# Performance work log

Measured on AMD Instinct MI355X. Metric: run time of the kernel, lower is better.

Reference implementation:

```python
import jax, jax.numpy as jnp
import numpy as np
from jax.scipy.special import logsumexp

T = 2048   # trajectory length
S = 512    # state dim (self.s)
B = 16     # number of options (self.b)
A = 18     # number of actions (self.a)
PEN = 0.5  # abstract_penalty
NEG = -1e9 # padding log-prob for not-yet-created option rows


def setup_inputs() -> dict:
    key = jax.random.key(0)
    k1, k2, k3, k4, k5 = jax.random.split(key, 5)
    s_i = jax.random.normal(k1, (T + 1, S), dtype=jnp.float32)
    W_action = jax.random.normal(k2, (S, B * A), dtype=jnp.float32) * 0.05
    W_stop = jax.random.normal(k3, (S, B * 2), dtype=jnp.float32) * 0.05
    W_start = jax.random.normal(k4, (S, B), dtype=jnp.float32) * 0.05
    actions = jax.random.randint(k5, (T,), 0, A, dtype=jnp.int64)
    return {"s_i": s_i, "W_action": W_action, "W_stop": W_stop,
            "W_start": W_start, "actions": actions}


def _hmm_logp(s_i, W_action, W_stop, W_start, actions):
    # abstract_policy_net: linear heads + log_softmax over the relevant axis
    action_logps = jax.nn.log_softmax((s_i @ W_action).reshape(T + 1, B, A), axis=-1)
    stop_logps = jax.nn.log_softmax((s_i @ W_stop).reshape(T + 1, B, 2), axis=-1)
    start_logps = jax.nn.log_softmax(s_i @ W_start, axis=-1)  # (T+1, B)

    # padded option_step_dist buffer: row i is created at step i (torch.cat append)
    buf0 = jnp.full((T, B), NEG, dtype=s_i.dtype).at[0].set(start_logps[0])

    def step(carry, xs):
        buf, tot = carry
        i, act = xs
        stop = stop_logps[i]          # (B, 2)
        start_lps = start_logps[i]    # (B,)
        # rearrange mass: options that stop get redistributed to new starts
        total_rearrange = logsumexp(buf + stop[:, 1]) - PEN
        new_mass = start_lps + total_rearrange
        buf2 = (buf + stop[:, 0]).at[i].set(new_mass)
        buf = jnp.where(i > 0, buf2, buf)  # i == 0 skips the rearrange branch
        action_lps = action_logps[i, :, act]  # (B,)
        tot = tot + logsumexp(action_lps + buf)
        return (buf, tot), None

    xs = (jnp.arange(T), actions)
    (buf, total_logp), _ = jax.lax.scan(step, (buf0, jnp.asarray(0.0, s_i.dtype)), xs)
    # final: all options must stop (note original uses index 0 here, as in source)
    total_logp = total_logp + logsumexp(stop_logps[-1, :, 0] + buf)
    return total_logp


def reference(s_i, W_action, W_stop, W_start, actions):
    return _hmm_logp(s_i, W_action, W_stop, W_start, actions)
```

## Files before the change

### kernel.cpp

```cpp
#include <hip/hip_runtime.h>

#define TT    2048
#define SS    512
#define NB    16
#define EPEN  0.60653065971263342f
#define NCHUNK 64
#define CLEN   32

typedef __attribute__((ext_vector_type(4))) float  floatx4;
typedef __attribute__((ext_vector_type(8))) short  bf16x8;

__device__ __forceinline__ ushort f2bf(float x) {
  unsigned u = __float_as_uint(x);
  u += 0x7fffu + ((u >> 16) & 1u);
  return (ushort)(u >> 16);
}

__device__ __forceinline__ unsigned pack2(ushort a, ushort b) {
  return (unsigned)a | ((unsigned)b << 16);
}

__global__ __launch_bounds__(256) void prep_kernel(
    const float* __restrict__ Wa, const float* __restrict__ Ws,
    const float* __restrict__ Wst, const float* __restrict__ s_i,
    ushort* __restrict__ Wt2, ushort* __restrict__ Af)
{
  int fid = blockIdx.x * 256 + threadIdx.x;
  if (fid < 21504) {
    const int q = fid & 3, rc = (fid >> 2) & 15, kt = (fid >> 6) & 15, colt = fid >> 10;
    const int col = colt * 16 + rc;
    const int kbase = kt * 32 + q * 8;
    ushort h[8];
    #pragma unroll
    for (int e = 0; e < 8; ++e) {
      const int k = kbase + e;
      float v;
      if (col < 288)      v = Wa [(size_t)k * 288 + col];
      else if (col < 320) v = Ws [(size_t)k * 32  + (col - 288)];
      else                v = Wst[(size_t)k * 16  + (col - 320)];
      h[e] = f2bf(v);
    }
    uint4 o = make_uint4(pack2(h[0], h[1]), pack2(h[2], h[3]),
                         pack2(h[4], h[5]), pack2(h[6], h[7]));
    *(uint4*)(Wt2 + (size_t)fid * 8) = o;
  } else {
    const int aid = fid - 21504;
    if (aid < 132096) {
      const int q = aid & 3, rc = (aid >> 2) & 15, kt = (aid >> 6) & 15, mt = aid >> 10;
      int row = mt * 16 + rc; if (row > TT) row = TT;
      const float* src = s_i + (size_t)row * SS + kt * 32 + q * 8;
      float4 v0 = *(const float4*)src;
      float4 v1 = *(const float4*)(src + 4);
      uint4 o = make_uint4(pack2(f2bf(v0.x), f2bf(v0.y)),
                           pack2(f2bf(v0.z), f2bf(v0.w)),
                           pack2(f2bf(v1.x), f2bf(v1.y)),
                           pack2(f2bf(v1.z), f2bf(v1.w)));
      *(uint4*)(Af + (size_t)aid * 8) = o;
    }
  }
}

__global__ __launch_bounds__(512) void proj_kernel(
    const ushort* __restrict__ Af,
    const ushort* __restrict__ Wt2,
    const int*   __restrict__ actions,
    float4*      __restrict__ coef)
{
  __shared__ float lg[16][346];

  const int tid  = threadIdx.x;
  const int wave = tid >> 6, lane = tid & 63;
  const int q = lane >> 4, rc = lane & 15;
  const int row0 = blockIdx.x * 16;

  const int kh = wave >> 2;
  const int ng = wave & 3;
  const int ntiles = (ng == 0) ? 6 : 5;
  const int kt0 = kh * 8;

  const ushort* aBase = Af  + (size_t)blockIdx.x * 8192 + rc * 32 + q * 8;
  const ushort* bBase = Wt2 + rc * 32 + q * 8;

  floatx4 acc[6];
  #pragma unroll
  for (int j = 0; j < 6; ++j) acc[j] = (floatx4)(0.f);

  bf16x8 aC, aN, bC[6], bN[6];

  aC = *(const bf16x8*)(aBase + kt0 * 512);
  #pragma unroll
  for (int j = 0; j < 6; ++j) {
    if (j < ntiles) {
      const int colt = ng + 4 * j;
      bC[j] = *(const bf16x8*)(bBase + (size_t)colt * 8192 + kt0 * 512);
    }
  }

  #pragma unroll
  for (int kk = 0; kk < 8; ++kk) {
    const int kt = kt0 + kk;
    if (kk < 7) {
      aN = *(const bf16x8*)(aBase + (kt + 1) * 512);
      #pragma unroll
      for (int j = 0; j < 6; ++j) {
        if (j < ntiles) {
          const int colt = ng + 4 * j;
          bN[j] = *(const bf16x8*)(bBase + (size_t)colt * 8192 + (kt + 1) * 512);
        }
      }
    }
    #pragma unroll
    for (int j = 0; j < 6; ++j) {
      if (j < ntiles)
        acc[j] = __builtin_amdgcn_mfma_f32_16x16x32_bf16(aC, bC[j], acc[j], 0, 0, 0);
    }
    aC = aN;
    #pragma unroll
    for (int j = 0; j < 6; ++j) {
      if (j < ntiles) bC[j] = bN[j];
    }
  }

  if (kh == 0) {
    #pragma unroll
    for (int j = 0; j < 6; ++j) {
      if (j < ntiles) {
        const int colt = ng + 4 * j;
        #pragma unroll
        for (int reg = 0; reg < 4; ++reg)
          lg[q * 4 + reg][colt * 16 + rc] = acc[j][reg];
      }
    }
  }
  __syncthreads();
  if (kh == 1) {
    #pragma unroll
    for (int j = 0; j < 6; ++j) {
      if (j < ntiles) {
        const int colt = ng + 4 * j;
        #pragma unroll
        for (int reg = 0; reg < 4; ++reg)
          lg[q * 4 + reg][colt * 16 + rc] += acc[j][reg];
      }
    }
  }
  __syncthreads();

  if (tid < 256) {
    const int r = tid >> 4, b = tid & 15;
    const int row = row0 + r;
    if (row < TT) {
      float m = -3.4e38f;
      #pragma unroll
      for (int a = 0; a < 18; ++a) m = fmaxf(m, lg[r][b * 18 + a]);
      float sum = 0.f;
      #pragma unroll
      for (int a = 0; a < 18; ++a) sum += __expf(lg[r][b * 18 + a] - m);
      int act = actions[row];
      float aprob = __expf(lg[r][b * 18 + act] - m) / sum;

      float x0 = lg[r][288 + 2 * b], x1 = lg[r][288 + 2 * b + 1];
      float mm = fmaxf(x0, x1);
      float e0 = __expf(x0 - mm), e1 = __expf(x1 - mm);
      float inv = 1.f / (e0 + e1);

      float ms = -3.4e38f;
      #pragma unroll
      for (int j = 0; j < 16; ++j) ms = fmaxf(ms, lg[r][320 + j]);
      float ssum = 0.f;
      #pragma unroll
      for (int j = 0; j < 16; ++j) ssum += __expf(lg[r][320 + j] - ms);
      float stp = __expf(lg[r][320 + b] - ms) / ssum;

      coef[(size_t)row * NB + b] = make_float4(e0 * inv, e1 * inv, stp, aprob);
    } else if (row == TT) {
      float x0 = lg[r][288 + 2 * b], x1 = lg[r][288 + 2 * b + 1];
      float mm = fmaxf(x0, x1);
      float e0 = __expf(x0 - mm), e1 = __expf(x1 - mm);
      coef[(size_t)TT * NB + b] = make_float4(1.f, 0.f, 0.f, e0 / (e0 + e1));
    }
  }
}

__global__ __launch_bounds__(64) void pass1_kernel(
    const float4* __restrict__ coef,
    float* __restrict__ Wws, float* __restrict__ Mws)
{
  const int chunk = blockIdx.x * 4 + (threadIdx.x >> 4);
  const int c = threadIdx.x & 15;
  const int i0 = chunk * CLEN + 1;

  float G[16];
  #pragma unroll
  for (int r = 0; r < 16; ++r) G[r] = (r == c) ? 1.f : 0.f;

  float4 cfA[16], cfB[16];
  #pragma unroll
  for (int r = 0; r < 16; ++r) cfA[r] = coef[(size_t)i0 * 16 + r];
  #pragma unroll
  for (int r = 0; r < 16; ++r) cfB[r] = coef[(size_t)(i0 + 1) * 16 + r];

#define P1BODY(CUR, NXT, J)                                                  \
  {                                                                          \
    if ((J) + 2 < CLEN) {                                                    \
      _Pragma("unroll")                                                      \
      for (int r = 0; r < 16; ++r)                                           \
        NXT[r] = coef[(size_t)(i0 + (J) + 2) * 16 + r];                      \
    }                                                                        \
    float ta = 0.f, tb = 0.f, tc = 0.f, td = 0.f;                            \
    _Pragma("unroll")                                                        \
    for (int r = 0; r < 4; ++r) {                                            \
      ta = fmaf(CUR[r].y,      G[r],      ta);                               \
      tb = fmaf(CUR[r + 4].y,  G[r + 4],  tb);                               \
      tc = fmaf(CUR[r + 8].y,  G[r + 8],  tc);                               \
      td = fmaf(CUR[r + 12].y, G[r + 12], td);                               \
    }                                                                        \
    float et = EPEN * ((ta + tb) + (tc + td));                               \
    _Pragma("unroll")                                                        \
    for (int r = 0; r < 16; ++r)                                             \
      G[r] = fmaf(CUR[r].x, G[r], CUR[r].z * et);                            \
    float wa = 0.f, wb = 0.f, wc = 0.f, wd = 0.f;                            \
    _Pragma("unroll")                                                        \
    for (int r = 0; r < 4; ++r) {                                            \
      wa = fmaf(CUR[r].w,      G[r],      wa);                               \
      wb = fmaf(CUR[r + 4].w,  G[r + 4],  wb);                               \
      wc = fmaf(CUR[r + 8].w,  G[r + 8],  wc);                               \
      wd = fmaf(CUR[r + 12].w, G[r + 12], wd);                               \
    }                                                                        \
    Wws[(size_t)(chunk * CLEN + (J)) * 16 + c] = (wa + wb) + (wc + wd);      \
  }

  for (int j = 0; j < CLEN; j += 2) {
    P1BODY(cfA, cfB, j);
    P1BODY(cfB, cfA, j + 1);
  }
#undef P1BODY

  #pragma unroll
  for (int r = 0; r < 16; ++r)
    Mws[chunk * 256 + r * 16 + c] = G[r];
}

__global__ __launch_bounds__(512) void pass2_kernel(
    const float4* __restrict__ coef,
    const float* __restrict__ Wws, const float* __restrict__ Mws,
    float* __restrict__ out)
{
  __shared__ float pbuf[NCHUNK][16];
  __shared__ float wacc[8];

  const int tid = threadIdx.x;
  long long Ktot = 0;

  if (tid < 64) {
    const int r = tid >> 2, g = tid & 3;
    float pj0 = coef[4 * g + 0].z;
    float pj1 = coef[4 * g + 1].z;
    float pj2 = coef[4 * g + 2].z;
    float pj3 = coef[4 * g + 3].z;

    const int moff = r * 16 + 4 * g;
    const int gb0 = 64 * g, gb1 = gb0 + 16, gb2 = gb0 + 32, gb3 = gb0 + 48;
    int Ecum = 0;

    float4 mR0 = *(const float4*)&Mws[0 * 256 + moff];
    float4 mR1 = *(const float4*)&Mws[1 * 256 + moff];
    float4 mR2 = *(const float4*)&Mws[2 * 256 + moff];
    float4 mR3 = *(const float4*)&Mws[3 * 256 + moff];
    float4 mR4 = *(const float4*)&Mws[4 * 256 + moff];
    float4 mR5 = *(const float4*)&Mws[5 * 256 + moff];
    float4 mR6 = *(const float4*)&Mws[6 * 256 + moff];
    float4 mR7 = *(const float4*)&Mws[7 * 256 + moff];

#define P2BODY(K, MREG, KPF)                                                 \
    {                                                                        \
      if (r == 0)                                                            \
        *(float4*)&pbuf[(K)][4 * g] = make_float4(pj0, pj1, pj2, pj3);       \
      Ktot += 32LL * (long long)Ecum;                                        \
      float part = fmaf(MREG.x, pj0,                                         \
                   fmaf(MREG.y, pj1, fmaf(MREG.z, pj2, MREG.w * pj3)));      \
      if ((KPF) < NCHUNK)                                                    \
        MREG = *(const float4*)&Mws[(KPF) * 256 + moff];                     \
              \
      part += __int_as_float(__builtin_amdgcn_mov_dpp(                       \
          __float_as_int(part), 0x39, 0xF, 0xF, true));      \
      part += __int_as_float(__builtin_amdgcn_mov_dpp(                       \
          __float_as_int(part), 0x4E, 0xF, 0xF, true));      \
      int ip = __float_as_int(part);                                         \
      float n0 = __int_as_float(__builtin_amdgcn_ds_bpermute(gb0, ip));      \
      float n1 = __int_as_float(__builtin_amdgcn_ds_bpermute(gb1, ip));      \
      float n2 = __int_as_float(__builtin_amdgcn_ds_bpermute(gb2, ip));      \
      float n3 = __int_as_float(__builtin_amdgcn_ds_bpermute(gb3, ip));      \
      int y0b = __builtin_amdgcn_readfirstlane(__float_as_int(n0));          \
      int eb = (y0b >> 23) & 255;                                            \
      Ecum += eb - 127;                                                      \
      float sc = __int_as_float((254 - eb) << 23);                           \
      pj0 = n0 * sc; pj1 = n1 * sc; pj2 = n2 * sc; pj3 = n3 * sc;            \
    }

    for (int kb = 0; kb < NCHUNK; kb += 8) {
      P2BODY(kb + 0, mR0, kb + 8);
      P2BODY(kb + 1, mR1, kb + 9);
      P2BODY(kb + 2, mR2, kb + 10);
      P2BODY(kb + 3, mR3, kb + 11);
      P2BODY(kb + 4, mR4, kb + 12);
      P2BODY(kb + 5, mR5, kb + 13);
      P2BODY(kb + 6, mR6, kb + 14);
      P2BODY(kb + 7, mR7, kb + 15);
    }
#undef P2BODY
  }
  __syncthreads();

  const int j0 = tid * 4;
  const int chunk = j0 >> 5;
  float p[16];
  #pragma unroll
  for (int c = 0; c < 16; ++c) p[c] = pbuf[chunk][c];

  float lacc = 0.f;
  #pragma unroll
  for (int jj = 0; jj < 4; ++jj) {
    const float* w = Wws + (size_t)(j0 + jj) * 16;
    float4 w0 = *(const float4*)(w);
    float4 w1 = *(const float4*)(w + 4);
    float4 w2 = *(const float4*)(w + 8);
    float4 w3 = *(const float4*)(w + 12);
    float s0 = fmaf(w0.x, p[0],  fmaf(w0.y, p[1],  fmaf(w0.z, p[2],  w0.w * p[3])));
    float s1 = fmaf(w1.x, p[4],  fmaf(w1.y, p[5],  fmaf(w1.z, p[6],  w1.w * p[7])));
    float s2 = fmaf(w2.x, p[8],  fmaf(w2.y, p[9],  fmaf(w2.z, p[10], w2.w * p[11])));
    float s3 = fmaf(w3.x, p[12], fmaf(w3.y, p[13], fmaf(w3.z, p[14], w3.w * p[15])));
    lacc += __logf((s0 + s1) + (s2 + s3));
  }

  if (tid == 0) {
    float U0 = 0.f;
    #pragma unroll
    for (int c = 0; c < 16; ++c) U0 = fmaf(coef[c].w, coef[c].z, U0);
    lacc += __logf(U0);
  }

  lacc += __shfl_xor(lacc, 1, 64);
  lacc += __shfl_xor(lacc, 2, 64);
  lacc += __shfl_xor(lacc, 4, 64);
  lacc += __shfl_xor(lacc, 8, 64);
  lacc += __shfl_xor(lacc, 16, 64);
  lacc += __shfl_xor(lacc, 32, 64);
  if ((tid & 63) == 0) wacc[tid >> 6] = lacc;
  __syncthreads();
  if (tid == 0) {
    double s = 0.0;
    #pragma unroll
    for (int i = 0; i < 8; ++i) s += (double)wacc[i];
    out[0] = (float)(s + 0.6931471805599453 * (double)Ktot);
  }
}

extern "C" void kernel_launch(void* const* d_in, const int* in_sizes, int n_in,
                              void* d_out, int out_size, void* d_ws, size_t ws_size,
                              hipStream_t stream) {
  const float* s_i = (const float*)d_in[0];
  const float* Wa  = (const float*)d_in[1];
  const float* Ws  = (const float*)d_in[2];
  const float* Wst = (const float*)d_in[3];
  const int*   act = (const int*)d_in[4];

  char* ws = (char*)d_ws;
  float4* coef = (float4*)ws;
  float*  Wws  = (float*)(ws + 524544);
  float*  Mws  = (float*)(ws + 524544 + 131072);
  ushort* Wt2  = (ushort*)(ws + 721152);
  ushort* Af   = (ushort*)(ws + 1065216);

  prep_kernel <<<600, 256, 0, stream>>>(Wa, Ws, Wst, s_i, Wt2, Af);
  proj_kernel <<<129, 512, 0, stream>>>(Af, Wt2, act, coef);
  pass1_kernel<<<16,  64,  0, stream>>>(coef, Wws, Mws);
  pass2_kernel<<<1,   512, 0, stream>>>(coef, Wws, Mws, (float*)d_out);
}
```

Measured before the change: 98.11 us.

## Fuse four kernels into one cooperative kernel with grid-wide syncs

Merges the prep, projection, pass1 and pass2 kernels into a single cooperative launch of 129 blocks, with grid.sync() separating the stages. The aim is to remove the per-kernel launch gaps between four small dependent kernels. In exchange, the prep stage now runs on fewer threads in a grid-stride loop, and each stage pays for a grid barrier. Cooperative launch also needs all blocks to be resident at once, which limits occupancy and the available shared memory per block.

```diff
diff --git a/kernel.cpp b/kernel.cpp
--- a/kernel.cpp
+++ b/kernel.cpp
@@ -1,4 +1,7 @@
 #include <hip/hip_runtime.h>
+#include <hip/hip_cooperative_groups.h>
+
+namespace cg = cooperative_groups;
 
 #define TT    2048
 #define SS    512
@@ -20,32 +23,44 @@
   return (unsigned)a | ((unsigned)b << 16);
 }
 
-__global__ __launch_bounds__(256) void prep_kernel(
-    const float* __restrict__ Wa, const float* __restrict__ Ws,
+__global__ __launch_bounds__(512) void mega_kernel(
+    const float* __restrict__ Wa,  const float* __restrict__ Ws,
     const float* __restrict__ Wst, const float* __restrict__ s_i,
-    ushort* __restrict__ Wt2, ushort* __restrict__ Af)
+    const int*   __restrict__ actions,
+    ushort* __restrict__ Wt2, ushort* __restrict__ Af,
+    float4* __restrict__ coef,
+    float*  __restrict__ Wws, float* __restrict__ Mws,
+    float*  __restrict__ out)
 {
-  int fid = blockIdx.x * 256 + threadIdx.x;
-  if (fid < 21504) {
-    const int q = fid & 3, rc = (fid >> 2) & 15, kt = (fid >> 6) & 15, colt = fid >> 10;
-    const int col = colt * 16 + rc;
-    const int kbase = kt * 32 + q * 8;
-    ushort h[8];
-    #pragma unroll
-    for (int e = 0; e < 8; ++e) {
-      const int k = kbase + e;
-      float v;
-      if (col < 288)      v = Wa [(size_t)k * 288 + col];
-      else if (col < 320) v = Ws [(size_t)k * 32  + (col - 288)];
-      else                v = Wst[(size_t)k * 16  + (col - 320)];
-      h[e] = f2bf(v);
-    }
-    uint4 o = make_uint4(pack2(h[0], h[1]), pack2(h[2], h[3]),
-                         pack2(h[4], h[5]), pack2(h[6], h[7]));
-    *(uint4*)(Wt2 + (size_t)fid * 8) = o;
-  } else {
-    const int aid = fid - 21504;
-    if (aid < 132096) {
+  cg::grid_group grid = cg::this_grid();
+
+  __shared__ float lg[16][346];
+  __shared__ float pbuf[NCHUNK][16];
+  __shared__ float wacc[8];
+
+  const int tid = threadIdx.x;
+  const int bid = blockIdx.x;
+
+  for (int fid = bid * 512 + tid; fid < 153600; fid += 129 * 512) {
+    if (fid < 21504) {
+      const int q = fid & 3, rc = (fid >> 2) & 15, kt = (fid >> 6) & 15, colt = fid >> 10;
+      const int col = colt * 16 + rc;
+      const int kbase = kt * 32 + q * 8;
+      ushort h[8];
+      #pragma unroll
+      for (int e = 0; e < 8; ++e) {
+        const int k = kbase + e;
+        float v;
+        if (col < 288)      v = Wa [(size_t)k * 288 + col];
+        else if (col < 320) v = Ws [(size_t)k * 32  + (col - 288)];
+        else                v = Wst[(size_t)k * 16  + (col - 320)];
+        h[e] = f2bf(v);
+      }
+      uint4 o = make_uint4(pack2(h[0], h[1]), pack2(h[2], h[3]),
+                           pack2(h[4], h[5]), pack2(h[6], h[7]));
+      *(uint4*)(Wt2 + (size_t)fid * 8) = o;
+    } else {
+      const int aid = fid - 21504;
       const int q = aid & 3, rc = (aid >> 2) & 15, kt = (aid >> 6) & 15, mt = aid >> 10;
       int row = mt * 16 + rc; if (row > TT) row = TT;
       const float* src = s_i + (size_t)row * SS + kt * 32 + q * 8;
@@ -58,301 +73,284 @@
       *(uint4*)(Af + (size_t)aid * 8) = o;
     }
   }
-}
-
-__global__ __launch_bounds__(512) void proj_kernel(
-    const ushort* __restrict__ Af,
-    const ushort* __restrict__ Wt2,
-    const int*   __restrict__ actions,
-    float4*      __restrict__ coef)
-{
-  __shared__ float lg[16][346];
-
-  const int tid  = threadIdx.x;
-  const int wave = tid >> 6, lane = tid & 63;
-  const int q = lane >> 4, rc = lane & 15;
-  const int row0 = blockIdx.x * 16;
-
-  const int kh = wave >> 2;
-  const int ng = wave & 3;
-  const int ntiles = (ng == 0) ? 6 : 5;
-  const int kt0 = kh * 8;
-
-  const ushort* aBase = Af  + (size_t)blockIdx.x * 8192 + rc * 32 + q * 8;
-  const ushort* bBase = Wt2 + rc * 32 + q * 8;
-
-  floatx4 acc[6];
-  #pragma unroll
-  for (int j = 0; j < 6; ++j) acc[j] = (floatx4)(0.f);
-
-  bf16x8 aC, aN, bC[6], bN[6];
-
-  aC = *(const bf16x8*)(aBase + kt0 * 512);
-  #pragma unroll
-  for (int j = 0; j < 6; ++j) {
-    if (j < ntiles) {
-      const int colt = ng + 4 * j;
-      bC[j] = *(const bf16x8*)(bBase + (size_t)colt * 8192 + kt0 * 512);
-    }
-  }
-
-  #pragma unroll
-  for (int kk = 0; kk < 8; ++kk) {
-    const int kt = kt0 + kk;
-    if (kk < 7) {
-      aN = *(const bf16x8*)(aBase + (kt + 1) * 512);
+  grid.sync();
+
+  {
+    const int wave = tid >> 6, lane = tid & 63;
+    const int q = lane >> 4, rc = lane & 15;
+    const int row0 = bid * 16;
+
+    const int kh = wave >> 2;
+    const int ng = wave & 3;
+    const int ntiles = (ng == 0) ? 6 : 5;
+    const int kt0 = kh * 8;
+
+    const ushort* aBase = Af  + (size_t)bid * 8192 + rc * 32 + q * 8;
+    const ushort* bBase = Wt2 + rc * 32 + q * 8;
+
+    floatx4 acc[6];
+    #pragma unroll
+    for (int j = 0; j < 6; ++j) acc[j] = (floatx4)(0.f);
+
+    bf16x8 aC, aN, bC[6], bN[6];
+
+    aC = *(const bf16x8*)(aBase + kt0 * 512);
+    #pragma unroll
+    for (int j = 0; j < 6; ++j) {
+      if (j < ntiles) {
+        const int colt = ng + 4 * j;
+        bC[j] = *(const bf16x8*)(bBase + (size_t)colt * 8192 + kt0 * 512);
+      }
+    }
+
+    #pragma unroll
+    for (int kk = 0; kk < 8; ++kk) {
+      const int kt = kt0 + kk;
+      if (kk < 7) {
+        aN = *(const bf16x8*)(aBase + (kt + 1) * 512);
+        #pragma unroll
+        for (int j = 0; j < 6; ++j) {
+          if (j < ntiles) {
+            const int colt = ng + 4 * j;
+            bN[j] = *(const bf16x8*)(bBase + (size_t)colt * 8192 + (kt + 1) * 512);
+          }
+        }
+      }
+      #pragma unroll
+      for (int j = 0; j < 6; ++j) {
+        if (j < ntiles)
+          acc[j] = __builtin_amdgcn_mfma_f32_16x16x32_bf16(aC, bC[j], acc[j], 0, 0, 0);
+      }
+      aC = aN;
+      #pragma unroll
+      for (int j = 0; j < 6; ++j) {
+        if (j < ntiles) bC[j] = bN[j];
+      }
+    }
+
+    if (kh == 0) {
       #pragma unroll
       for (int j = 0; j < 6; ++j) {
         if (j < ntiles) {
           const int colt = ng + 4 * j;
-          bN[j] = *(const bf16x8*)(bBase + (size_t)colt * 8192 + (kt + 1) * 512);
+          #pragma unroll
+          for (int reg = 0; reg < 4; ++reg)
+            lg[q * 4 + reg][colt * 16 + rc] = acc[j][reg];
         }
       }
     }
-    #pragma unroll
-    for (int j = 0; j < 6; ++j) {
-      if (j < ntiles)
-        acc[j] = __builtin_amdgcn_mfma_f32_16x16x32_bf16(aC, bC[j], acc[j], 0, 0, 0);
-    }
-    aC = aN;
-    #pragma unroll
-    for (int j = 0; j < 6; ++j) {
-      if (j < ntiles) bC[j] = bN[j];
+    __syncthreads();
+    if (kh == 1) {
+      #pragma unroll
+      for (int j = 0; j < 6; ++j) {
+        if (j < ntiles) {
+          const int colt = ng + 4 * j;
+          #pragma unroll
+          for (int reg = 0; reg < 4; ++reg)
+            lg[q * 4 + reg][colt * 16 + rc] += acc[j][reg];
+        }
+      }
+    }
+    __syncthreads();
+
+    if (tid < 256) {
+      const int r = tid >> 4, b = tid & 15;
+      const int row = row0 + r;
+      if (row < TT) {
+        float m = -3.4e38f;
+        #pragma unroll
+        for (int a = 0; a < 18; ++a) m = fmaxf(m, lg[r][b * 18 + a]);
+        float sum = 0.f;
+        #pragma unroll
+        for (int a = 0; a < 18; ++a) sum += __expf(lg[r][b * 18 + a] - m);
+        int act = actions[row];
+        float aprob = __expf(lg[r][b * 18 + act] - m) / sum;
+
+        float x0 = lg[r][288 + 2 * b], x1 = lg[r][288 + 2 * b + 1];
+        float mm = fmaxf(x0, x1);
+        float e0 = __expf(x0 - mm), e1 = __expf(x1 - mm);
+        float inv = 1.f / (e0 + e1);
+
+        float ms = -3.4e38f;
+        #pragma unroll
+        for (int j = 0; j < 16; ++j) ms = fmaxf(ms, lg[r][320 + j]);
+        float ssum = 0.f;
+        #pragma unroll
+        for (int j = 0; j < 16; ++j) ssum += __expf(lg[r][320 + j] - ms);
+        float stp = __expf(lg[r][320 + b] - ms) / ssum;
+
+        coef[(size_t)row * NB + b] = make_float4(e0 * inv, e1 * inv, stp, aprob);
+      } else if (row == TT) {
+        float x0 = lg[r][288 + 2 * b], x1 = lg[r][288 + 2 * b + 1];
+        float mm = fmaxf(x0, x1);
+        float e0 = __expf(x0 - mm), e1 = __expf(x1 - mm);
+        coef[(size_t)TT * NB + b] = make_float4(1.f, 0.f, 0.f, e0 / (e0 + e1));
+      }
     }
   }
-
-  if (kh == 0) {
-    #pragma unroll
-    for (int j = 0; j < 6; ++j) {
-      if (j < ntiles) {
-        const int colt = ng + 4 * j;
-        #pragma unroll
-        for (int reg = 0; reg < 4; ++reg)
-          lg[q * 4 + reg][colt * 16 + rc] = acc[j][reg];
-      }
-    }
-  }
-  __syncthreads();
-  if (kh == 1) {
-    #pragma unroll
-    for (int j = 0; j < 6; ++j) {
-      if (j < ntiles) {
-        const int colt = ng + 4 * j;
-        #pragma unroll
-        for (int reg = 0; reg < 4; ++reg)
-          lg[q * 4 + reg][colt * 16 + rc] += acc[j][reg];
-      }
-    }
-  }
-  __syncthreads();
-
-  if (tid < 256) {
-    const int r = tid >> 4, b = tid & 15;
-    const int row = row0 + r;
-    if (row < TT) {
-      float m = -3.4e38f;
-      #pragma unroll
-      for (int a = 0; a < 18; ++a) m = fmaxf(m, lg[r][b * 18 + a]);
-      float sum = 0.f;
-      #pragma unroll
-      for (int a = 0; a < 18; ++a) sum += __expf(lg[r][b * 18 + a] - m);
-      int act = actions[row];
-      float aprob = __expf(lg[r][b * 18 + act] - m) / sum;
-
-      float x0 = lg[r][288 + 2 * b], x1 = lg[r][288 + 2 * b + 1];
-      float mm = fmaxf(x0, x1);
-      float e0 = __expf(x0 - mm), e1 = __expf(x1 - mm);
-      float inv = 1.f / (e0 + e1);
-
-      float ms = -3.4e38f;
-      #pragma unroll
-      for (int j = 0; j < 16; ++j) ms = fmaxf(ms, lg[r][320 + j]);
-      float ssum = 0.f;
-      #pragma unroll
-      for (int j = 0; j < 16; ++j) ssum += __expf(lg[r][320 + j] - ms);
-      float stp = __expf(lg[r][320 + b] - ms) / ssum;
-
-      coef[(size_t)row * NB + b] = make_float4(e0 * inv, e1 * inv, stp, aprob);
-    } else if (row == TT) {
-      float x0 = lg[r][288 + 2 * b], x1 = lg[r][288 + 2 * b + 1];
-      float mm = fmaxf(x0, x1);
-      float e0 = __expf(x0 - mm), e1 = __expf(x1 - mm);
-      coef[(size_t)TT * NB + b] = make_float4(1.f, 0.f, 0.f, e0 / (e0 + e1));
-    }
-  }
-}
-
-__global__ __launch_bounds__(64) void pass1_kernel(
-    const float4* __restrict__ coef,
-    float* __restrict__ Wws, float* __restrict__ Mws)
-{
-  const int chunk = blockIdx.x * 4 + (threadIdx.x >> 4);
-  const int c = threadIdx.x & 15;
-  const int i0 = chunk * CLEN + 1;
-
-  float G[16];
-  #pragma unroll
-  for (int r = 0; r < 16; ++r) G[r] = (r == c) ? 1.f : 0.f;
-
-  float4 cfA[16], cfB[16];
-  #pragma unroll
-  for (int r = 0; r < 16; ++r) cfA[r] = coef[(size_t)i0 * 16 + r];
-  #pragma unroll
-  for (int r = 0; r < 16; ++r) cfB[r] = coef[(size_t)(i0 + 1) * 16 + r];
+  grid.sync();
+
+  if (bid < 16 && tid < 64) {
+    const int chunk = bid * 4 + (tid >> 4);
+    const int c = tid & 15;
+    const int i0 = chunk * CLEN + 1;
+
+    float G[16];
+    #pragma unroll
+    for (int r = 0; r < 16; ++r) G[r] = (r == c) ? 1.f : 0.f;
+
+    float4 cfA[16], cfB[16];
+    #pragma unroll
+    for (int r = 0; r < 16; ++r) cfA[r] = coef[(size_t)i0 * 16 + r];
+    #pragma unroll
+    for (int r = 0; r < 16; ++r) cfB[r] = coef[(size_t)(i0 + 1) * 16 + r];
 
 #define P1BODY(CUR, NXT, J)                                                  \
-  {                                                                          \
-    if ((J) + 2 < CLEN) {                                                    \
+    {                                                                        \
+      if ((J) + 2 < CLEN) {                                                  \
+        _Pragma("unroll")                                                    \
+        for (int r = 0; r < 16; ++r)                                         \
+          NXT[r] = coef[(size_t)(i0 + (J) + 2) * 16 + r];                    \
+      }                                                                      \
+      float ta = 0.f, tb = 0.f, tc = 0.f, td = 0.f;                          \
+      _Pragma("unroll")                                                      \
+      for (int r = 0; r < 4; ++r) {                                          \
+        ta = fmaf(CUR[r].y,      G[r],      ta);                             \
+        tb = fmaf(CUR[r + 4].y,  G[r + 4],  tb);                             \
+        tc = fmaf(CUR[r + 8].y,  G[r + 8],  tc);                             \
+        td = fmaf(CUR[r + 12].y, G[r + 12], td);                             \
+      }                                                                      \
+      float et = EPEN * ((ta + tb) + (tc + td));                             \
       _Pragma("unroll")                                                      \
       for (int r = 0; r < 16; ++r)                                           \
-        NXT[r] = coef[(size_t)(i0 + (J) + 2) * 16 + r];                      \
-    }                                                                        \
-    float ta = 0.f, tb = 0.f, tc = 0.f, td = 0.f;                            \
-    _Pragma("unroll")                                                        \
-    for (int r = 0; r < 4; ++r) {                                            \
-      ta = fmaf(CUR[r].y,      G[r],      ta);                               \
-      tb = fmaf(CUR[r + 4].y,  G[r + 4],  tb);                               \
-      tc = fmaf(CUR[r + 8].y,  G[r + 8],  tc);                               \
-      td = fmaf(CUR[r + 12].y, G[r + 12], td);                               \
-    }                                                                        \
-    float et = EPEN * ((ta + tb) + (tc + td));                               \
-    _Pragma("unroll")                                                        \
-    for (int r = 0; r < 16; ++r)                                             \
-      G[r] = fmaf(CUR[r].x, G[r], CUR[r].z * et);                            \
-    float wa = 0.f, wb = 0.f, wc = 0.f, wd = 0.f;                            \
-    _Pragma("unroll")                                                        \
-    for (int r = 0; r < 4; ++r) {                                            \
-      wa = fmaf(CUR[r].w,      G[r],      wa);                               \
-      wb = fmaf(CUR[r + 4].w,  G[r + 4],  wb);                               \
-      wc = fmaf(CUR[r + 8].w,  G[r + 8],  wc);                               \
-      wd = fmaf(CUR[r + 12].w, G[r + 12], wd);                               \
-    }                                                                        \
-    Wws[(size_t)(chunk * CLEN + (J)) * 16 + c] = (wa + wb) + (wc + wd);      \
+        G[r] = fmaf(CUR[r].x, G[r], CUR[r].z * et);                          \
+      float wa = 0.f, wb = 0.f, wc = 0.f, wd = 0.f;                          \
+      _Pragma("unroll")                                                      \
+      for (int r = 0; r < 4; ++r) {                                          \
+        wa = fmaf(CUR[r].w,      G[r],      wa);                             \
+        wb = fmaf(CUR[r + 4].w,  G[r + 4],  wb);                             \
+        wc = fmaf(CUR[r + 8].w,  G[r + 8],  wc);                             \
+        wd = fmaf(CUR[r + 12].w, G[r + 12], wd);                             \
+      }                                                                      \
+      Wws[(size_t)(chunk * CLEN + (J)) * 16 + c] = (wa + wb) + (wc + wd);    \
+    }
+
+    for (int j = 0; j < CLEN; j += 2) {
+      P1BODY(cfA, cfB, j);
+      P1BODY(cfB, cfA, j + 1);
+    }
+#undef P1BODY
+
+    #pragma unroll
+    for (int r = 0; r < 16; ++r)
+      Mws[chunk * 256 + r * 16 + c] = G[r];
   }
-
-  for (int j = 0; j < CLEN; j += 2) {
-    P1BODY(cfA, cfB, j);
-    P1BODY(cfB, cfA, j + 1);
-  }
-#undef P1BODY
-
-  #pragma unroll
-  for (int r = 0; r < 16; ++r)
-    Mws[chunk * 256 + r * 16 + c] = G[r];
-}
-
-__global__ __launch_bounds__(512) void pass2_kernel(
-    const float4* __restrict__ coef,
-    const float* __restrict__ Wws, const float* __restrict__ Mws,
-    float* __restrict__ out)
-{
-  __shared__ float pbuf[NCHUNK][16];
-  __shared__ float wacc[8];
-
-  const int tid = threadIdx.x;
-  long long Ktot = 0;
-
-  if (tid < 64) {
-    const int r = tid >> 2, g = tid & 3;
-    float pj0 = coef[4 * g + 0].z;
-    float pj1 = coef[4 * g + 1].z;
-    float pj2 = coef[4 * g + 2].z;
-    float pj3 = coef[4 * g + 3].z;
-
-    const int moff = r * 16 + 4 * g;
-    const int gb0 = 64 * g, gb1 = gb0 + 16, gb2 = gb0 + 32, gb3 = gb0 + 48;
-    int Ecum = 0;
-
-    float4 mR0 = *(const float4*)&Mws[0 * 256 + moff];
-    float4 mR1 = *(const float4*)&Mws[1 * 256 + moff];
-    float4 mR2 = *(const float4*)&Mws[2 * 256 + moff];
-    float4 mR3 = *(const float4*)&Mws[3 * 256 + moff];
-    float4 mR4 = *(const float4*)&Mws[4 * 256 + moff];
-    float4 mR5 = *(const float4*)&Mws[5 * 256 + moff];
-    float4 mR6 = *(const float4*)&Mws[6 * 256 + moff];
-    float4 mR7 = *(const float4*)&Mws[7 * 256 + moff];
+  grid.sync();
+
+  if (bid == 0) {
+    long long Ktot = 0;
+
+    if (tid < 64) {
+      const int r = tid >> 2, g = tid & 3;
+      float pj0 = coef[4 * g + 0].z;
+      float pj1 = coef[4 * g + 1].z;
+      float pj2 = coef[4 * g + 2].z;
+      float pj3 = coef[4 * g + 3].z;
+
+      const int moff = r * 16 + 4 * g;
+      const int gb0 = 64 * g, gb1 = gb0 + 16, gb2 = gb0 + 32, gb3 = gb0 + 48;
+      int Ecum = 0;
+
+      float4 mR0 = *(const float4*)&Mws[0 * 256 + moff];
+      float4 mR1 = *(const float4*)&Mws[1 * 256 + moff];
+      float4 mR2 = *(const float4*)&Mws[2 * 256 + moff];
+      float4 mR3 = *(const float4*)&Mws[3 * 256 + moff];
+      float4 mR4 = *(const float4*)&Mws[4 * 256 + moff];
+      float4 mR5 = *(const float4*)&Mws[5 * 256 + moff];
+      float4 mR6 = *(const float4*)&Mws[6 * 256 + moff];
+      float4 mR7 = *(const float4*)&Mws[7 * 256 + moff];
 
 #define P2BODY(K, MREG, KPF)                                                 \
-    {                                                                        \
-      if (r == 0)                                                            \
-        *(float4*)&pbuf[(K)][4 * g] = make_float4(pj0, pj1, pj2, pj3);       \
-      Ktot += 32LL * (long long)Ecum;                                        \
-      float part = fmaf(MREG.x, pj0,                                         \
-                   fmaf(MREG.y, pj1, fmaf(MREG.z, pj2, MREG.w * pj3)));      \
-      if ((KPF) < NCHUNK)                                                    \
-        MREG = *(const float4*)&Mws[(KPF) * 256 + moff];                     \
-              \
-      part += __int_as_float(__builtin_amdgcn_mov_dpp(                       \
-          __float_as_int(part), 0x39, 0xF, 0xF, true));      \
-      part += __int_as_float(__builtin_amdgcn_mov_dpp(                       \
-          __float_as_int(part), 0x4E, 0xF, 0xF, true));      \
-      int ip = __float_as_int(part);                                         \
-      float n0 = __int_as_float(__builtin_amdgcn_ds_bpermute(gb0, ip));      \
-      float n1 = __int_as_float(__builtin_amdgcn_ds_bpermute(gb1, ip));      \
-      float n2 = __int_as_float(__builtin_amdgcn_ds_bpermute(gb2, ip));      \
-      float n3 = __int_as_float(__builtin_amdgcn_ds_bpermute(gb3, ip));      \
-      int y0b = __builtin_amdgcn_readfirstlane(__float_as_int(n0));          \
-      int eb = (y0b >> 23) & 255;                                            \
-      Ecum += eb - 127;                                                      \
-      float sc = __int_as_float((254 - eb) << 23);                           \
-      pj0 = n0 * sc; pj1 = n1 * sc; pj2 = n2 * sc; pj3 = n3 * sc;            \
-    }
-
-    for (int kb = 0; kb < NCHUNK; kb += 8) {
-      P2BODY(kb + 0, mR0, kb + 8);
-      P2BODY(kb + 1, mR1, kb + 9);
-      P2BODY(kb + 2, mR2, kb + 10);
-      P2BODY(kb + 3, mR3, kb + 11);
-      P2BODY(kb + 4, mR4, kb + 12);
-      P2BODY(kb + 5, mR5, kb + 13);
-      P2BODY(kb + 6, mR6, kb + 14);
-      P2BODY(kb + 7, mR7, kb + 15);
-    }
+      {                                                                      \
+        if (r == 0)                                                          \
+          *(float4*)&pbuf[(K)][4 * g] = make_float4(pj0, pj1, pj2, pj3);     \
+        Ktot += 32LL * (long long)Ecum;                                      \
+        float part = fmaf(MREG.x, pj0,                                       \
+                     fmaf(MREG.y, pj1, fmaf(MREG.z, pj2, MREG.w * pj3)));    \
+        if ((KPF) < NCHUNK)                                                  \
+          MREG = *(const float4*)&Mws[(KPF) * 256 + moff];                   \
+        part += __int_as_float(__builtin_amdgcn_mov_dpp(                     \
+            __float_as_int(part), 0x39, 0xF, 0xF, true));    \
+        part += __int_as_float(__builtin_amdgcn_mov_dpp(                     \
+            __float_as_int(part), 0x4E, 0xF, 0xF, true));    \
+        int ip = __float_as_int(part);                                       \
+        float n0 = __int_as_float(__builtin_amdgcn_ds_bpermute(gb0, ip));    \
+        float n1 = __int_as_float(__builtin_amdgcn_ds_bpermute(gb1, ip));    \
+        float n2 = __int_as_float(__builtin_amdgcn_ds_bpermute(gb2, ip));    \
+        float n3 = __int_as_float(__builtin_amdgcn_ds_bpermute(gb3, ip));    \
+        int y0b = __builtin_amdgcn_readfirstlane(__float_as_int(n0));        \
+        int eb = (y0b >> 23) & 255;                                          \
+        Ecum += eb - 127;                                                    \
+        float sc = __int_as_float((254 - eb) << 23);                         \
+        pj0 = n0 * sc; pj1 = n1 * sc; pj2 = n2 * sc; pj3 = n3 * sc;          \
+      }
+
+      for (int kb = 0; kb < NCHUNK; kb += 8) {
+        P2BODY(kb + 0, mR0, kb + 8);
+        P2BODY(kb + 1, mR1, kb + 9);
+        P2BODY(kb + 2, mR2, kb + 10);
+        P2BODY(kb + 3, mR3, kb + 11);
+        P2BODY(kb + 4, mR4, kb + 12);
+        P2BODY(kb + 5, mR5, kb + 13);
+        P2BODY(kb + 6, mR6, kb + 14);
+        P2BODY(kb + 7, mR7, kb + 15);
+      }
 #undef P2BODY
-  }
-  __syncthreads();
-
-  const int j0 = tid * 4;
-  const int chunk = j0 >> 5;
-  float p[16];
-  #pragma unroll
-  for (int c = 0; c < 16; ++c) p[c] = pbuf[chunk][c];
-
-  float lacc = 0.f;
-  #pragma unroll
-  for (int jj = 0; jj < 4; ++jj) {
-    const float* w = Wws + (size_t)(j0 + jj) * 16;
-    float4 w0 = *(const float4*)(w);
-    float4 w1 = *(const float4*)(w + 4);
-    float4 w2 = *(const float4*)(w + 8);
-    float4 w3 = *(const float4*)(w + 12);
-    float s0 = fmaf(w0.x, p[0],  fmaf(w0.y, p[1],  fmaf(w0.z, p[2],  w0.w * p[3])));
-    float s1 = fmaf(w1.x, p[4],  fmaf(w1.y, p[5],  fmaf(w1.z, p[6],  w1.w * p[7])));
-    float s2 = fmaf(w2.x, p[8],  fmaf(w2.y, p[9],  fmaf(w2.z, p[10], w2.w * p[11])));
-    float s3 = fmaf(w3.x, p[12], fmaf(w3.y, p[13], fmaf(w3.z, p[14], w3.w * p[15])));
-    lacc += __logf((s0 + s1) + (s2 + s3));
-  }
-
-  if (tid == 0) {
-    float U0 = 0.f;
-    #pragma unroll
-    for (int c = 0; c < 16; ++c) U0 = fmaf(coef[c].w, coef[c].z, U0);
-    lacc += __logf(U0);
-  }
-
-  lacc += __shfl_xor(lacc, 1, 64);
-  lacc += __shfl_xor(lacc, 2, 64);
-  lacc += __shfl_xor(lacc, 4, 64);
-  lacc += __shfl_xor(lacc, 8, 64);
-  lacc += __shfl_xor(lacc, 16, 64);
-  lacc += __shfl_xor(lacc, 32, 64);
-  if ((tid & 63) == 0) wacc[tid >> 6] = lacc;
-  __syncthreads();
-  if (tid == 0) {
-    double s = 0.0;
-    #pragma unroll
-    for (int i = 0; i < 8; ++i) s += (double)wacc[i];
-    out[0] = (float)(s + 0.6931471805599453 * (double)Ktot);
+    }
+    __syncthreads();
+
+    const int j0 = tid * 4;
+    const int chunk = j0 >> 5;
+    float p[16];
+    #pragma unroll
+    for (int c = 0; c < 16; ++c) p[c] = pbuf[chunk][c];
+
+    float lacc = 0.f;
+    #pragma unroll
+    for (int jj = 0; jj < 4; ++jj) {
+      const float* w = Wws + (size_t)(j0 + jj) * 16;
+      float4 w0 = *(const float4*)(w);
+      float4 w1 = *(const float4*)(w + 4);
+      float4 w2 = *(const float4*)(w + 8);
+      float4 w3 = *(const float4*)(w + 12);
+      float s0 = fmaf(w0.x, p[0],  fmaf(w0.y, p[1],  fmaf(w0.z, p[2],  w0.w * p[3])));
+      float s1 = fmaf(w1.x, p[4],  fmaf(w1.y, p[5],  fmaf(w1.z, p[6],  w1.w * p[7])));
+      float s2 = fmaf(w2.x, p[8],  fmaf(w2.y, p[9],  fmaf(w2.z, p[10], w2.w * p[11])));
+      float s3 = fmaf(w3.x, p[12], fmaf(w3.y, p[13], fmaf(w3.z, p[14], w3.w * p[15])));
+      lacc += __logf((s0 + s1) + (s2 + s3));
+    }
+
+    if (tid == 0) {
+      float U0 = 0.f;
+      #pragma unroll
+      for (int c = 0; c < 16; ++c) U0 = fmaf(coef[c].w, coef[c].z, U0);
+      lacc += __logf(U0);
+    }
+
+    lacc += __shfl_xor(lacc, 1, 64);
+    lacc += __shfl_xor(lacc, 2, 64);
+    lacc += __shfl_xor(lacc, 4, 64);
+    lacc += __shfl_xor(lacc, 8, 64);
+    lacc += __shfl_xor(lacc, 16, 64);
+    lacc += __shfl_xor(lacc, 32, 64);
+    if ((tid & 63) == 0) wacc[tid >> 6] = lacc;
+    __syncthreads();
+    if (tid == 0) {
+      double s = 0.0;
+      #pragma unroll
+      for (int i = 0; i < 8; ++i) s += (double)wacc[i];
+      out[0] = (float)(s + 0.6931471805599453 * (double)Ktot);
+    }
   }
 }
 
@@ -371,9 +369,13 @@
   float*  Mws  = (float*)(ws + 524544 + 131072);
   ushort* Wt2  = (ushort*)(ws + 721152);
   ushort* Af   = (ushort*)(ws + 1065216);
-
-  prep_kernel <<<600, 256, 0, stream>>>(Wa, Ws, Wst, s_i, Wt2, Af);
-  proj_kernel <<<129, 512, 0, stream>>>(Af, Wt2, act, coef);
-  pass1_kernel<<<16,  64,  0, stream>>>(coef, Wws, Mws);
-  pass2_kernel<<<1,   512, 0, stream>>>(coef, Wws, Mws, (float*)d_out);
+  float*  outp = (float*)d_out;
+
+  void* args[] = {
+    (void*)&Wa, (void*)&Ws, (void*)&Wst, (void*)&s_i, (void*)&act,
+    (void*)&Wt2, (void*)&Af, (void*)&coef, (void*)&Wws, (void*)&Mws,
+    (void*)&outp
+  };
+  hipLaunchCooperativeKernel((const void*)mega_kernel,
+                             dim3(129), dim3(512), args, 0, stream);
 }
```

New measurement: 156.2 us. 59.2% more time.

## Fuse activation bf16 conversion into projection and merge scan passes into one kernel

Applied to the files above, without the earlier changes.

Activation bf16 conversion moves from the prep kernel into the projection kernel, which stages its 16-row tile in shared memory. The two scan passes become one single-block kernel that keeps the chunk transfer matrices in LDS rather than a global workspace, cutting one launch and a round trip. The exponent-broadcast readfirstlane becomes a ds_bpermute from lane 0. The cost is that pass1 now runs in one block (512 threads, two rounds) instead of 16 blocks, which serialises that work.

```diff
diff --git a/kernel.cpp b/kernel.cpp
--- a/kernel.cpp
+++ b/kernel.cpp
@@ -22,50 +22,35 @@
 
 __global__ __launch_bounds__(256) void prep_kernel(
     const float* __restrict__ Wa, const float* __restrict__ Ws,
-    const float* __restrict__ Wst, const float* __restrict__ s_i,
-    ushort* __restrict__ Wt2, ushort* __restrict__ Af)
+    const float* __restrict__ Wst, ushort* __restrict__ Wt2)
 {
   int fid = blockIdx.x * 256 + threadIdx.x;
-  if (fid < 21504) {
-    const int q = fid & 3, rc = (fid >> 2) & 15, kt = (fid >> 6) & 15, colt = fid >> 10;
-    const int col = colt * 16 + rc;
-    const int kbase = kt * 32 + q * 8;
-    ushort h[8];
-    #pragma unroll
-    for (int e = 0; e < 8; ++e) {
-      const int k = kbase + e;
-      float v;
-      if (col < 288)      v = Wa [(size_t)k * 288 + col];
-      else if (col < 320) v = Ws [(size_t)k * 32  + (col - 288)];
-      else                v = Wst[(size_t)k * 16  + (col - 320)];
-      h[e] = f2bf(v);
-    }
-    uint4 o = make_uint4(pack2(h[0], h[1]), pack2(h[2], h[3]),
-                         pack2(h[4], h[5]), pack2(h[6], h[7]));
-    *(uint4*)(Wt2 + (size_t)fid * 8) = o;
-  } else {
-    const int aid = fid - 21504;
-    if (aid < 132096) {
-      const int q = aid & 3, rc = (aid >> 2) & 15, kt = (aid >> 6) & 15, mt = aid >> 10;
-      int row = mt * 16 + rc; if (row > TT) row = TT;
-      const float* src = s_i + (size_t)row * SS + kt * 32 + q * 8;
-      float4 v0 = *(const float4*)src;
-      float4 v1 = *(const float4*)(src + 4);
-      uint4 o = make_uint4(pack2(f2bf(v0.x), f2bf(v0.y)),
-                           pack2(f2bf(v0.z), f2bf(v0.w)),
-                           pack2(f2bf(v1.x), f2bf(v1.y)),
-                           pack2(f2bf(v1.z), f2bf(v1.w)));
-      *(uint4*)(Af + (size_t)aid * 8) = o;
-    }
-  }
+  if (fid >= 21504) return;
+  const int q = fid & 3, rc = (fid >> 2) & 15, kt = (fid >> 6) & 15, colt = fid >> 10;
+  const int col = colt * 16 + rc;
+  const int kbase = kt * 32 + q * 8;
+  ushort h[8];
+  #pragma unroll
+  for (int e = 0; e < 8; ++e) {
+    const int k = kbase + e;
+    float v;
+    if (col < 288)      v = Wa [(size_t)k * 288 + col];
+    else if (col < 320) v = Ws [(size_t)k * 32  + (col - 288)];
+    else                v = Wst[(size_t)k * 16  + (col - 320)];
+    h[e] = f2bf(v);
+  }
+  uint4 o = make_uint4(pack2(h[0], h[1]), pack2(h[2], h[3]),
+                       pack2(h[4], h[5]), pack2(h[6], h[7]));
+  *(uint4*)(Wt2 + (size_t)fid * 8) = o;
 }
 
 __global__ __launch_bounds__(512) void proj_kernel(
-    const ushort* __restrict__ Af,
+    const float* __restrict__ s_i,
     const ushort* __restrict__ Wt2,
     const int*   __restrict__ actions,
     float4*      __restrict__ coef)
 {
+  __shared__ __align__(16) ushort At[8192];
   __shared__ float lg[16][346];
 
   const int tid  = threadIdx.x;
@@ -73,12 +58,28 @@
   const int q = lane >> 4, rc = lane & 15;
   const int row0 = blockIdx.x * 16;
 
+  #pragma unroll
+  for (int u = 0; u < 2; ++u) {
+    const int uid = tid + u * 512;
+    const int qq = uid & 3, rr = (uid >> 2) & 15, kt = uid >> 6;
+    int row = row0 + rr; if (row > TT) row = TT;
+    const float* src = s_i + (size_t)row * SS + kt * 32 + qq * 8;
+    float4 v0 = *(const float4*)src;
+    float4 v1 = *(const float4*)(src + 4);
+    uint4 o = make_uint4(pack2(f2bf(v0.x), f2bf(v0.y)),
+                         pack2(f2bf(v0.z), f2bf(v0.w)),
+                         pack2(f2bf(v1.x), f2bf(v1.y)),
+                         pack2(f2bf(v1.z), f2bf(v1.w)));
+    *(uint4*)(At + (size_t)uid * 8) = o;
+  }
+  __syncthreads();
+
   const int kh = wave >> 2;
   const int ng = wave & 3;
   const int ntiles = (ng == 0) ? 6 : 5;
   const int kt0 = kh * 8;
 
-  const ushort* aBase = Af  + (size_t)blockIdx.x * 8192 + rc * 32 + q * 8;
+  const ushort* aBase = At  + rc * 32 + q * 8;
   const ushort* bBase = Wt2 + rc * 32 + q * 8;
 
   floatx4 acc[6];
@@ -182,75 +183,74 @@
   }
 }
 
-__global__ __launch_bounds__(64) void pass1_kernel(
+__global__ __launch_bounds__(512) void pass12_kernel(
     const float4* __restrict__ coef,
-    float* __restrict__ Wws, float* __restrict__ Mws)
+    float* __restrict__ Wws,
+    float* __restrict__ out)
 {
-  const int chunk = blockIdx.x * 4 + (threadIdx.x >> 4);
-  const int c = threadIdx.x & 15;
-  const int i0 = chunk * CLEN + 1;
-
-  float G[16];
-  #pragma unroll
-  for (int r = 0; r < 16; ++r) G[r] = (r == c) ? 1.f : 0.f;
-
-  float4 cfA[16], cfB[16];
-  #pragma unroll
-  for (int r = 0; r < 16; ++r) cfA[r] = coef[(size_t)i0 * 16 + r];
-  #pragma unroll
-  for (int r = 0; r < 16; ++r) cfB[r] = coef[(size_t)(i0 + 1) * 16 + r];
+  __shared__ float Mlds[NCHUNK * 256];
+  __shared__ float pbuf[NCHUNK][16];
+  __shared__ float wacc[8];
+
+  const int tid = threadIdx.x;
+  long long Ktot = 0;
+
+  for (int round = 0; round < 2; ++round) {
+    const int chunk = (tid >> 4) + round * 32;
+    const int c = tid & 15;
+    const int i0 = chunk * CLEN + 1;
+
+    float G[16];
+    #pragma unroll
+    for (int r = 0; r < 16; ++r) G[r] = (r == c) ? 1.f : 0.f;
+
+    float4 cfA[16], cfB[16];
+    #pragma unroll
+    for (int r = 0; r < 16; ++r) cfA[r] = coef[(size_t)i0 * 16 + r];
+    #pragma unroll
+    for (int r = 0; r < 16; ++r) cfB[r] = coef[(size_t)(i0 + 1) * 16 + r];
 
 #define P1BODY(CUR, NXT, J)                                                  \
-  {                                                                          \
-    if ((J) + 2 < CLEN) {                                                    \
+    {                                                                        \
+      if ((J) + 2 < CLEN) {                                                  \
+        _Pragma("unroll")                                                    \
+        for (int r = 0; r < 16; ++r)                                         \
+          NXT[r] = coef[(size_t)(i0 + (J) + 2) * 16 + r];                    \
+      }                                                                      \
+      float ta = 0.f, tb = 0.f, tc = 0.f, td = 0.f;                          \
+      _Pragma("unroll")                                                      \
+      for (int r = 0; r < 4; ++r) {                                          \
+        ta = fmaf(CUR[r].y,      G[r],      ta);                             \
+        tb = fmaf(CUR[r + 4].y,  G[r + 4],  tb);                             \
+        tc = fmaf(CUR[r + 8].y,  G[r + 8],  tc);                             \
+        td = fmaf(CUR[r + 12].y, G[r + 12], td);                             \
+      }                                                                      \
+      float et = EPEN * ((ta + tb) + (tc + td));                             \
       _Pragma("unroll")                                                      \
       for (int r = 0; r < 16; ++r)                                           \
-        NXT[r] = coef[(size_t)(i0 + (J) + 2) * 16 + r];                      \
-    }                                                                        \
-    float ta = 0.f, tb = 0.f, tc = 0.f, td = 0.f;                            \
-    _Pragma("unroll")                                                        \
-    for (int r = 0; r < 4; ++r) {                                            \
-      ta = fmaf(CUR[r].y,      G[r],      ta);                               \
-      tb = fmaf(CUR[r + 4].y,  G[r + 4],  tb);                               \
-      tc = fmaf(CUR[r + 8].y,  G[r + 8],  tc);                               \
-      td = fmaf(CUR[r + 12].y, G[r + 12], td);                               \
-    }                                                                        \
-    float et = EPEN * ((ta + tb) + (tc + td));                               \
-    _Pragma("unroll")                                                        \
-    for (int r = 0; r < 16; ++r)                                             \
-      G[r] = fmaf(CUR[r].x, G[r], CUR[r].z * et);                            \
-    float wa = 0.f, wb = 0.f, wc = 0.f, wd = 0.f;                            \
-    _Pragma("unroll")                                                        \
-    for (int r = 0; r < 4; ++r) {                                            \
-      wa = fmaf(CUR[r].w,      G[r],      wa);                               \
-      wb = fmaf(CUR[r + 4].w,  G[r + 4],  wb);                               \
-      wc = fmaf(CUR[r + 8].w,  G[r + 8],  wc);                               \
-      wd = fmaf(CUR[r + 12].w, G[r + 12], wd);                               \
-    }                                                                        \
-    Wws[(size_t)(chunk * CLEN + (J)) * 16 + c] = (wa + wb) + (wc + wd);      \
-  }
-
-  for (int j = 0; j < CLEN; j += 2) {
-    P1BODY(cfA, cfB, j);
-    P1BODY(cfB, cfA, j + 1);
-  }
+        G[r] = fmaf(CUR[r].x, G[r], CUR[r].z * et);                          \
+      float wa = 0.f, wb = 0.f, wc = 0.f, wd = 0.f;                          \
+      _Pragma("unroll")                                                      \
+      for (int r = 0; r < 4; ++r) {                                          \
+        wa = fmaf(CUR[r].w,      G[r],      wa);                             \
+        wb = fmaf(CUR[r + 4].w,  G[r + 4],  wb);                             \
+        wc = fmaf(CUR[r + 8].w,  G[r + 8],  wc);                             \
+        wd = fmaf(CUR[r + 12].w, G[r + 12], wd);                             \
+      }                                                                      \
+      Wws[(size_t)(chunk * CLEN + (J)) * 16 + c] = (wa + wb) + (wc + wd);    \
+    }
+
+    for (int j = 0; j < CLEN; j += 2) {
+      P1BODY(cfA, cfB, j);
+      P1BODY(cfB, cfA, j + 1);
+    }
 #undef P1BODY
 
-  #pragma unroll
-  for (int r = 0; r < 16; ++r)
-    Mws[chunk * 256 + r * 16 + c] = G[r];
-}
-
-__global__ __launch_bounds__(512) void pass2_kernel(
-    const float4* __restrict__ coef,
-    const float* __restrict__ Wws, const float* __restrict__ Mws,
-    float* __restrict__ out)
-{
-  __shared__ float pbuf[NCHUNK][16];
-  __shared__ float wacc[8];
-
-  const int tid = threadIdx.x;
-  long long Ktot = 0;
+    #pragma unroll
+    for (int r = 0; r < 16; ++r)
+      Mlds[chunk * 256 + r * 16 + c] = G[r];
+  }
+  __syncthreads();
 
   if (tid < 64) {
     const int r = tid >> 2, g = tid & 3;
@@ -263,14 +263,14 @@
     const int gb0 = 64 * g, gb1 = gb0 + 16, gb2 = gb0 + 32, gb3 = gb0 + 48;
     int Ecum = 0;
 
-    float4 mR0 = *(const float4*)&Mws[0 * 256 + moff];
-    float4 mR1 = *(const float4*)&Mws[1 * 256 + moff];
-    float4 mR2 = *(const float4*)&Mws[2 * 256 + moff];
-    float4 mR3 = *(const float4*)&Mws[3 * 256 + moff];
-    float4 mR4 = *(const float4*)&Mws[4 * 256 + moff];
-    float4 mR5 = *(const float4*)&Mws[5 * 256 + moff];
-    float4 mR6 = *(const float4*)&Mws[6 * 256 + moff];
-    float4 mR7 = *(const float4*)&Mws[7 * 256 + moff];
+    float4 mR0 = *(const float4*)&Mlds[0 * 256 + moff];
+    float4 mR1 = *(const float4*)&Mlds[1 * 256 + moff];
+    float4 mR2 = *(const float4*)&Mlds[2 * 256 + moff];
+    float4 mR3 = *(const float4*)&Mlds[3 * 256 + moff];
+    float4 mR4 = *(const float4*)&Mlds[4 * 256 + moff];
+    float4 mR5 = *(const float4*)&Mlds[5 * 256 + moff];
+    float4 mR6 = *(const float4*)&Mlds[6 * 256 + moff];
+    float4 mR7 = *(const float4*)&Mlds[7 * 256 + moff];
 
 #define P2BODY(K, MREG, KPF)                                                 \
     {                                                                        \
@@ -280,8 +280,8 @@
       float part = fmaf(MREG.x, pj0,                                         \
                    fmaf(MREG.y, pj1, fmaf(MREG.z, pj2, MREG.w * pj3)));      \
       if ((KPF) < NCHUNK)                                                    \
-        MREG = *(const float4*)&Mws[(KPF) * 256 + moff];                     \
-              \
+        MREG = *(const float4*)&Mlds[(KPF) * 256 + moff];                    \
+                                 \
       part += __int_as_float(__builtin_amdgcn_mov_dpp(                       \
           __float_as_int(part), 0x39, 0xF, 0xF, true));      \
       part += __int_as_float(__builtin_amdgcn_mov_dpp(                       \
@@ -291,8 +291,8 @@
       float n1 = __int_as_float(__builtin_amdgcn_ds_bpermute(gb1, ip));      \
       float n2 = __int_as_float(__builtin_amdgcn_ds_bpermute(gb2, ip));      \
       float n3 = __int_as_float(__builtin_amdgcn_ds_bpermute(gb3, ip));      \
-      int y0b = __builtin_amdgcn_readfirstlane(__float_as_int(n0));          \
-      int eb = (y0b >> 23) & 255;                                            \
+      float y0 = __int_as_float(__builtin_amdgcn_ds_bpermute(0,   ip));      \
+      int eb = (__float_as_int(y0) >> 23) & 255;                             \
       Ecum += eb - 127;                                                      \
       float sc = __int_as_float((254 - eb) << 23);                           \
       pj0 = n0 * sc; pj1 = n1 * sc; pj2 = n2 * sc; pj3 = n3 * sc;            \
@@ -368,12 +368,9 @@
   char* ws = (char*)d_ws;
   float4* coef = (float4*)ws;
   float*  Wws  = (float*)(ws + 524544);
-  float*  Mws  = (float*)(ws + 524544 + 131072);
-  ushort* Wt2  = (ushort*)(ws + 721152);
-  ushort* Af   = (ushort*)(ws + 1065216);
-
-  prep_kernel <<<600, 256, 0, stream>>>(Wa, Ws, Wst, s_i, Wt2, Af);
-  proj_kernel <<<129, 512, 0, stream>>>(Af, Wt2, act, coef);
-  pass1_kernel<<<16,  64,  0, stream>>>(coef, Wws, Mws);
-  pass2_kernel<<<1,   512, 0, stream>>>(coef, Wws, Mws, (float*)d_out);
-}
+  ushort* Wt2  = (ushort*)(ws + 524544 + 131072);
+
+  prep_kernel  <<<84,  256, 0, stream>>>(Wa, Ws, Wst, Wt2);
+  proj_kernel  <<<129, 512, 0, stream>>>(s_i, Wt2, act, coef);
+  pass12_kernel<<<1,   512, 0, stream>>>(coef, Wws, (float*)d_out);
+}
```

Result: slower. 140.6 us (+43.3%).
